# Performance work log

Measured on AMD Instinct MI355X. Metric: run time of the kernel, lower is better.

The kernel has to match this reference:

```python
import jax, jax.numpy as jnp
import numpy as np

EPS = 1e-5


def _conv(x, w, groups=1):
    # x: NCHW, w: OIHW, stride 1, padding k//2 == SAME for k=3
    return jax.lax.conv_general_dilated(
        x, w, window_strides=(1, 1), padding='SAME',
        feature_group_count=groups,
        dimension_numbers=('NCHW', 'OIHW', 'NCHW'))


def _bn(x, gamma, beta, mean, var):
    # eval-mode BatchNorm2d
    s = gamma * jax.lax.rsqrt(var + EPS)
    return x * s[None, :, None, None] + (beta - mean * s)[None, :, None, None]


def _bilinear_up_kernel(ch, k):
    # dla_up.fill_up_weights: bilinear upsampling kernel, shape (ch, 1, k, k)
    f = (k + 1) // 2
    c = (2 * f - 1 - f % 2) / (2.0 * f)
    i = np.arange(k)
    w1d = 1.0 - np.abs(i / f - c)
    w2d = np.outer(w1d, w1d).astype(np.float32)  # (k, k)
    return jnp.asarray(np.broadcast_to(w2d, (ch, 1, k, k)).copy())


def setup_inputs() -> dict:
    key = jax.random.key(0)
    ks = jax.random.split(key, 8)
    B, C, H, W = 16, 32, 128, 128
    OUT, NL = 8, 4
    layers = jax.random.normal(ks[0], (NL + 1, B, C, H, W), jnp.float32)
    node_w = jax.random.normal(ks[1], (NL, C, 2 * C, 3, 3), jnp.float32) * 0.05
    node_gamma = jnp.ones((NL, C), jnp.float32)
    node_beta = jnp.zeros((NL, C), jnp.float32)
    node_mean = jax.random.normal(ks[2], (NL, C), jnp.float32) * 0.1
    node_var = jax.random.uniform(ks[3], (NL, C), jnp.float32, 0.5, 1.5)
    final_w = jax.random.normal(ks[4], (OUT, C, 3, 3), jnp.float32) * 0.05
    final_gamma = jnp.ones((OUT,), jnp.float32)
    final_beta = jnp.zeros((OUT,), jnp.float32)
    final_mean = jax.random.normal(ks[5], (OUT,), jnp.float32) * 0.1
    final_var = jax.random.uniform(ks[6], (OUT,), jnp.float32, 0.5, 1.5)
    up_w = _bilinear_up_kernel(OUT, 4)  # frozen depthwise transpose-conv weight
    return dict(layers=layers, node_w=node_w, node_gamma=node_gamma,
                node_beta=node_beta, node_mean=node_mean, node_var=node_var,
                final_w=final_w, final_gamma=final_gamma, final_beta=final_beta,
                final_mean=final_mean, final_var=final_var, up_w=up_w)


def reference(layers, node_w, node_gamma, node_beta, node_mean, node_var,
              final_w, final_gamma, final_beta, final_mean, final_var, up_w):
    x = layers[0]
    n_layers = node_w.shape[0]
    for i in range(n_layers):  # fixed small structural loop
        h = jnp.concatenate([x, layers[i + 1]], axis=1)  # [B, 2C, H, W]
        x = jax.nn.relu(_bn(_conv(h, node_w[i]),
                            node_gamma[i], node_beta[i], node_mean[i], node_var[i]))
    x = jnp.tanh(_bn(_conv(x, final_w),
                     final_gamma, final_beta, final_mean, final_var))
    # depthwise ConvTranspose2d(k=4, stride=2, pad=1): equivalent fractionally
    # strided conv with flipped kernel, lhs_dilation=2, padding k-1-pad=2
    groups = up_w.shape[0]
    x = jax.lax.conv_general_dilated(
        x, up_w[:, :, ::-1, ::-1], window_strides=(1, 1),
        padding=[(2, 2), (2, 2)], lhs_dilation=(2, 2),
        feature_group_count=groups,
        dimension_numbers=('NCHW', 'OIHW', 'NCHW'))  # [B, OUT, 2H, 2W]
    # vectorized form of the per-row / per-col delta loops
    Ho, Wo = x.shape[2], x.shape[3]
    row_ramp = jnp.arange(Ho, dtype=x.dtype) / Ho  # delta_i = i / H
    col_ramp = jnp.arange(Wo, dtype=x.dtype) / Wo  # delta_j = j / W
    x = x.at[:, 0].add(row_ramp[None, :, None])
    x = x.at[:, 1].add(col_ramp[None, None, :])
    return x
```

## Files before the change

kernel.cpp:

```cpp
#include <hip/hip_runtime.h>
#include <hip/hip_bf16.h>
#include <cmath>

using bf16 = __hip_bfloat16;
typedef _Float16 f16x8 __attribute__((ext_vector_type(8)));
typedef float f32x16 __attribute__((ext_vector_type(16)));

__device__ __forceinline__ float ldin(const void* p, size_t i, int f) {
    return f ? ((const float*)p)[i] : __bfloat162float(((const bf16*)p)[i]);
}

__device__ __forceinline__ float bfu(unsigned short u) {
    union { unsigned u32; float f; } x; x.u32 = (unsigned)u << 16; return x.f;
}

__device__ __forceinline__ int swq(int X) { return (X + (X >> 2)) & 3; }

__device__ __forceinline__ int detect_f(const void* layers_) {
    const unsigned short* u = (const unsigned short*)layers_;
    __shared__ int s_bad;
    if (threadIdx.x == 0) s_bad = 0;
    __syncthreads();
    int bad = 0;
#pragma unroll
    for (int k = 0; k < 16; ++k) {
        unsigned short v = u[2 * ((threadIdx.x * 16 + k) * 257)];
        int e = (v >> 7) & 0xFF;
        bad += (e == 0xFF || (e == 0 && (v & 0x7FFF))) ? 1 : 0;
    }
    if (bad) atomicAdd(&s_bad, bad);
    __syncthreads();
    return s_bad > 0;
}

__global__ void pack_kernel(const void* __restrict__ nw, const void* __restrict__ ng,
                            const void* __restrict__ nb, const void* __restrict__ nm,
                            const void* __restrict__ nv, const void* __restrict__ fw,
                            const void* __restrict__ fg, const void* __restrict__ fb,
                            const void* __restrict__ fm, const void* __restrict__ fv,
                            const void* __restrict__ upw, const void* __restrict__ layers_,
                            char* __restrict__ ws) {
    const int f = detect_f(layers_);
    if (blockIdx.x == 0 && threadIdx.x == 0) *(volatile int*)ws = f;
    int i = blockIdx.x * 256 + threadIdx.x;
    _Float16* wpkN = (_Float16*)(ws + 160);
    _Float16* wpkF = (_Float16*)(ws + 147616);
    float* upwf  = (float*)(ws + 166048);
    float* nbias = (float*)(ws + 166560);
    float* fbias = (float*)(ws + 167072);
    if (i < 73728) {
        int e = i & 7, lane = (i >> 3) & 63, rest = i >> 9;
        int t = rest % 9, rest2 = rest / 9;
        int kc = rest2 & 3, lay = rest2 >> 2;
        int oc = lane & 31, ic = kc * 16 + ((lane >> 5) << 3) + e;
        float s = ldin(ng, lay * 32 + oc, f) * rsqrtf(ldin(nv, lay * 32 + oc, f) + 1e-5f);
        float w = ldin(nw, ((size_t)(lay * 32 + oc) * 64 + ic) * 9 + t, f);
        wpkN[i] = (_Float16)(w * s);
    } else if (i < 82944) {
        int j = i - 73728;
        int e = j & 7, lane = (j >> 3) & 63, rest = j >> 9;
        int t = rest % 9, kc = rest / 9;
        int oc = lane & 31, ic = kc * 16 + ((lane >> 5) << 3) + e;
        float v = 0.f;
        if (oc < 8) {
            float s = ldin(fg, oc, f) * rsqrtf(ldin(fv, oc, f) + 1e-5f);
            v = ldin(fw, ((size_t)(oc * 32 + ic)) * 9 + t, f) * s;
        }
        wpkF[j] = (_Float16)v;
    } else if (i < 83072) {
        int k = i - 82944;
        upwf[k] = ldin(upw, k, f);
    } else if (i < 83200) {
        int k = i - 83072;
        float s = ldin(ng, k, f) * rsqrtf(ldin(nv, k, f) + 1e-5f);
        nbias[k] = ldin(nb, k, f) - ldin(nm, k, f) * s;
    } else if (i < 83232) {
        int k = i - 83200;
        float v = 0.f;
        if (k < 8) {
            float s = ldin(fg, k, f) * rsqrtf(ldin(fv, k, f) + 1e-5f);
            v = ldin(fb, k, f) - ldin(fm, k, f) * s;
        }
        fbias[k] = v;
    }
}

__device__ __forceinline__ void stage_nchw_g(char* lds, const void* src,
                                             size_t base_elem, int f, int tid,
                                             int x0g, int y0g) {
#pragma unroll
    for (int it = 0; it < 6; ++it) {
        int job = tid + it * 256;
        if (it < 5 || job < 1360) {
            int c = job / 340, rest = job - c * 340;
            int row = rest / 34, X = rest - row * 34;
            int gy = y0g - 1 + row, gx = x0g - 1 + X;
            union { _Float16 h[8]; uint4 v; } pk;
            if (gy >= 0 && gy < 128 && gx >= 0 && gx < 128) {
                size_t e0 = base_elem + (size_t)(c * 8) * 16384 + (size_t)gy * 128 + gx;
                if (f) {
#pragma unroll
                    for (int j = 0; j < 8; ++j)
                        pk.h[j] = (_Float16)(((const float*)src)[e0 + (size_t)j * 16384]);
                } else {
#pragma unroll
                    for (int j = 0; j < 8; ++j)
                        pk.h[j] = (_Float16)bfu(((const unsigned short*)src)[e0 + (size_t)j * 16384]);
                }
            } else {
                pk.v = make_uint4(0u, 0u, 0u, 0u);
            }
            int slot = (c + swq(X)) & 3;
            *(uint4*)(lds + row * 2176 + (X << 6) + (slot << 4)) = pk.v;
        }
    }
}

__device__ __forceinline__ void stage_nhwc(char* lds, const _Float16* xh, int tid,
                                           int b, int x0g, int y0g) {
#pragma unroll
    for (int it = 0; it < 6; ++it) {
        int q = tid + it * 256;
        if (it < 5 || q < 1360) {
            int p = q >> 2, s = q & 3;
            int row = p / 34, X = p - row * 34;
            int c = (s - swq(X)) & 3;
            int gy = y0g - 1 + row, gx = x0g - 1 + X;
            uint4 v = {0u, 0u, 0u, 0u};
            if (gy >= 0 && gy < 128 && gx >= 0 && gx < 128)
                v = *(const uint4*)(xh + (((size_t)(b * 128 + gy) * 128 + gx) * 32 + c * 8));
            *(uint4*)(lds + (q << 4)) = v;
        }
    }
}

__device__ __forceinline__ void conv_both(const char* lds, const _Float16* wseg,
                                          int lane, int wid, int lh,
                                          f32x16& acc0, f32x16& acc1) {
    const int l31 = lane & 31;
#pragma unroll
    for (int kc = 0; kc < 4; ++kc) {
        f16x8 bfr[9];
#pragma unroll
        for (int t = 0; t < 9; ++t)
            bfr[t] = *(const f16x8*)(wseg + (size_t)((kc * 9 + t) * 64 + lane) * 8);
        const char* pl = lds + ((kc & 2) ? 21760 : 0);
        const int chunk = ((kc & 1) << 1) | lh;
#pragma unroll
        for (int iy = 0; iy < 4; ++iy) {
            const int rowoff = ((wid << 1) + iy) * 2176;
#pragma unroll
            for (int kx = 0; kx < 3; ++kx) {
                const int X = l31 + kx;
                const int slot = (chunk + swq(X)) & 3;
                const f16x8 a = *(const f16x8*)(pl + rowoff + (X << 6) + (slot << 4));
#pragma unroll
                for (int ky = 0; ky < 3; ++ky) {
                    const int y = iy - ky;
                    if (y == 0)
                        acc0 = __builtin_amdgcn_mfma_f32_32x32x16_f16(a, bfr[ky * 3 + kx], acc0, 0, 0, 0);
                    else if (y == 1)
                        acc1 = __builtin_amdgcn_mfma_f32_32x32x16_f16(a, bfr[ky * 3 + kx], acc1, 0, 0, 0);
                }
            }
        }
    }
}

__device__ __forceinline__ void conv_plane(const char* lds, const _Float16* wseg,
                                           int lane, int wid, int lh,
                                           f32x16& acc0, f32x16& acc1) {
    const int l31 = lane & 31;
#pragma unroll
    for (int kc = 0; kc < 2; ++kc) {
        f16x8 bfr[9];
#pragma unroll
        for (int t = 0; t < 9; ++t)
            bfr[t] = *(const f16x8*)(wseg + (size_t)((kc * 9 + t) * 64 + lane) * 8);
        const int chunk = (kc << 1) | lh;
#pragma unroll
        for (int iy = 0; iy < 4; ++iy) {
            const int rowoff = ((wid << 1) + iy) * 2176;
#pragma unroll
            for (int kx = 0; kx < 3; ++kx) {
                const int X = l31 + kx;
                const int slot = (chunk + swq(X)) & 3;
                const f16x8 a = *(const f16x8*)(lds + rowoff + (X << 6) + (slot << 4));
#pragma unroll
                for (int ky = 0; ky < 3; ++ky) {
                    const int y = iy - ky;
                    if (y == 0)
                        acc0 = __builtin_amdgcn_mfma_f32_32x32x16_f16(a, bfr[ky * 3 + kx], acc0, 0, 0, 0);
                    else if (y == 1)
                        acc1 = __builtin_amdgcn_mfma_f32_32x32x16_f16(a, bfr[ky * 3 + kx], acc1, 0, 0, 0);
                }
            }
        }
    }
}

__global__ __launch_bounds__(256, 3) void node_conv_mfma(
    const void* __restrict__ xprev, int xprev_nchw, int xprev_slice,
    const void* __restrict__ layers, int skip_slice,
    const _Float16* __restrict__ wl, const float* __restrict__ bias,
    const int* __restrict__ flag, _Float16* __restrict__ out) {
    __shared__ char lds[43520];
    const int f = flag[0];
    const int tid = threadIdx.x;
    const int x0g = blockIdx.x << 5, y0g = blockIdx.y << 3, b = blockIdx.z;
    const int lane = tid & 63, wid = tid >> 6;
    const int l31 = lane & 31, lh = lane >> 5;

    if (xprev_nchw)
        stage_nchw_g(lds, xprev, (size_t)xprev_slice * 8388608 + (size_t)b * 524288,
                     f, tid, x0g, y0g);
    else
        stage_nhwc(lds, (const _Float16*)xprev, tid, b, x0g, y0g);
    stage_nchw_g(lds + 21760, layers, (size_t)skip_slice * 8388608 + (size_t)b * 524288,
                 f, tid, x0g, y0g);
    __syncthreads();

    f32x16 acc0, acc1;
#pragma unroll
    for (int r = 0; r < 16; ++r) { acc0[r] = 0.f; acc1[r] = 0.f; }
    conv_both(lds, wl, lane, wid, lh, acc0, acc1);
    __syncthreads();

    const float bs = bias[l31];
    const int row0 = wid << 1;
#pragma unroll
    for (int r = 0; r < 16; ++r) {
        const int xr = (r & 3) + ((r >> 2) << 3) + (lh << 2);
        *(_Float16*)(lds + (row0 * 32 + xr) * 80 + (l31 << 1)) =
            (_Float16)fmaxf(acc0[r] + bs, 0.f);
        *(_Float16*)(lds + ((row0 + 1) * 32 + xr) * 80 + (l31 << 1)) =
            (_Float16)fmaxf(acc1[r] + bs, 0.f);
    }
    __syncthreads();
    const size_t obase = ((size_t)(b * 128 + y0g) * 128 + x0g) * 32;
#pragma unroll
    for (int it = 0; it < 4; ++it) {
        int g = tid + it * 256;
        int prow = g >> 7, inrow = g & 127;
        uint4 v = *(const uint4*)(lds + (prow * 32 + (inrow >> 2)) * 80 + (inrow & 3) * 16);
        *(uint4*)(out + obase + (size_t)prow * 4096 + inrow * 8) = v;
    }
}

__device__ __forceinline__ float ftanh(float x) {
    float e = __expf(2.f * x);
    return 1.f - 2.f / (e + 1.f);
}

__global__ __launch_bounds__(256, 3) void final_conv_mfma(
    const _Float16* __restrict__ xin, const _Float16* __restrict__ wf,
    const float* __restrict__ fbias, _Float16* __restrict__ outF) {
    __shared__ char lds[21760];
    const int tid = threadIdx.x;
    const int x0g = blockIdx.x << 5, y0g = blockIdx.y << 3, b = blockIdx.z;
    const int lane = tid & 63, wid = tid >> 6;
    const int l31 = lane & 31, lh = lane >> 5;

    stage_nhwc(lds, xin, tid, b, x0g, y0g);
    __syncthreads();

    f32x16 acc0, acc1;
#pragma unroll
    for (int r = 0; r < 16; ++r) { acc0[r] = 0.f; acc1[r] = 0.f; }
    conv_plane(lds, wf, lane, wid, lh, acc0, acc1);
    __syncthreads();

    const float bs = fbias[l31];
    const int row0 = wid << 1;
    if (l31 < 8) {
#pragma unroll
        for (int r = 0; r < 16; ++r) {
            const int xr = (r & 3) + ((r >> 2) << 3) + (lh << 2);
            *(_Float16*)(lds + (row0 * 32 + xr) * 16 + (l31 << 1)) =
                (_Float16)ftanh(acc0[r] + bs);
            *(_Float16*)(lds + ((row0 + 1) * 32 + xr) * 16 + (l31 << 1)) =
                (_Float16)ftanh(acc1[r] + bs);
        }
    }
    __syncthreads();
    {
        int g = tid;
        int prow = g >> 5, px = g & 31;
        uint4 v = *(const uint4*)(lds + g * 16);
        *(uint4*)(outF + ((size_t)(b * 128 + y0g + prow) * 128 + x0g + px) * 8) = v;
    }
}

__global__ __launch_bounds__(256) void upsample_q(
    const _Float16* __restrict__ F, const float* __restrict__ wf,
    const int* __restrict__ flag, void* __restrict__ out) {
    const int f = flag[0];
    int i = blockIdx.x * 256 + threadIdx.x;
    int qx = i & 127, qy = (i >> 7) & 127, b = i >> 14;

    f16x8 inb[3][3];
#pragma unroll
    for (int jy = 0; jy < 3; ++jy)
#pragma unroll
        for (int jx = 0; jx < 3; ++jx) {
            int iy = qy - 1 + jy, ix = qx - 1 + jx;
            f16x8 v;
#pragma unroll
            for (int c = 0; c < 8; ++c) v[c] = (_Float16)0.f;
            if (iy >= 0 && iy < 128 && ix >= 0 && ix < 128)
                v = *(const f16x8*)(F + (((size_t)(b * 128 + iy) * 128 + ix) << 3));
            inb[jy][jx] = v;
        }

    float acc[32];
#pragma unroll
    for (int k = 0; k < 32; ++k) acc[k] = 0.f;
#pragma unroll
    for (int ky = 0; ky < 4; ++ky) {
        const int dy = 1 - (ky & 1), jy = 2 - ((ky + 1) >> 1);
#pragma unroll
        for (int kx = 0; kx < 4; ++kx) {
            const int dx = 1 - (kx & 1), jx = 2 - ((kx + 1) >> 1);
            const f16x8 p = inb[jy][jx];
#pragma unroll
            for (int c = 0; c < 8; ++c)
                acc[c * 4 + dy * 2 + dx] =
                    fmaf((float)p[c], wf[c * 16 + ky * 4 + kx], acc[c * 4 + dy * 2 + dx]);
        }
    }
#pragma unroll
    for (int d = 0; d < 4; ++d) {
        acc[d]     += (float)(2 * qy + (d >> 1)) * (1.0f / 256.0f);
        acc[4 + d] += (float)(2 * qx + (d & 1)) * (1.0f / 256.0f);
    }
#pragma unroll
    for (int c = 0; c < 8; ++c)
#pragma unroll
        for (int dy2 = 0; dy2 < 2; ++dy2) {
            size_t a = ((size_t)(b * 8 + c) * 256 + (qy * 2 + dy2)) * 256 + qx * 2;
            float v0 = acc[c * 4 + dy2 * 2], v1 = acc[c * 4 + dy2 * 2 + 1];
            if (f) {
                *(float2*)((float*)out + a) = make_float2(v0, v1);
            } else {
                union { bf16 h; unsigned short u; } u0, u1;
                u0.h = __float2bfloat16(v0); u1.h = __float2bfloat16(v1);
                ((unsigned*)out)[a >> 1] = (unsigned)u0.u | ((unsigned)u1.u << 16);
            }
        }
}

extern "C" void kernel_launch(void* const* d_in, const int* in_sizes, int n_in,
                              void* d_out, int out_size, void* d_ws, size_t ws_size,
                              hipStream_t stream) {
    const void* layers = d_in[0];
    const void* node_w = d_in[1];
    const void* ng     = d_in[2];
    const void* nb     = d_in[3];
    const void* nm     = d_in[4];
    const void* nv     = d_in[5];
    const void* fw     = d_in[6];
    const void* fg     = d_in[7];
    const void* fb     = d_in[8];
    const void* fm     = d_in[9];
    const void* fv     = d_in[10];
    const void* upw    = d_in[11];

    char* ws = (char*)d_ws;
    int* dflag       = (int*)d_ws;
    _Float16* wpkN   = (_Float16*)(ws + 160);
    _Float16* wpkF   = (_Float16*)(ws + 147616);
    float* upwf      = (float*)(ws + 166048);
    float* nbias     = (float*)(ws + 166560);
    float* fbias     = (float*)(ws + 167072);
    _Float16* X      = (_Float16*)(ws + 167424);
    _Float16* Y      = (_Float16*)d_out;

    pack_kernel<<<326, 256, 0, stream>>>(node_w, ng, nb, nm, nv,
                                         fw, fg, fb, fm, fv, upw, layers, ws);

    dim3 g(4, 16, 16), blk(256);
    node_conv_mfma<<<g, blk, 0, stream>>>(layers, 1, 0, layers, 1,
                                          wpkN, nbias, dflag, X);
    node_conv_mfma<<<g, blk, 0, stream>>>(X, 0, 0, layers, 2,
                                          wpkN + 18432, nbias + 32, dflag, Y);
    node_conv_mfma<<<g, blk, 0, stream>>>(Y, 0, 0, layers, 3,
                                          wpkN + 2 * 18432, nbias + 64, dflag, X);
    node_conv_mfma<<<g, blk, 0, stream>>>(X, 0, 0, layers, 4,
                                          wpkN + 3 * 18432, nbias + 96, dflag, Y);
    final_conv_mfma<<<g, blk, 0, stream>>>(Y, wpkF, fbias, X);
    upsample_q<<<1024, 256, 0, stream>>>(X, upwf, dflag, d_out);
}
```

Before: 388.8 us.

## Fuse all stages into a persistent megakernel with software grid barriers

Replaces the pack, four node-conv, final-conv and upsample launches with one persistent kernel of 512 blocks. Each block walks the 1024 tiles of every stage in a grid-stride loop, and stages are separated by an atomic-counter grid barrier in the workspace. Format detection now runs in every block instead of being stored as a flag. The aim is to remove per-launch overhead and the gaps between kernels. In exchange, each CU runs fewer concurrent blocks (2 instead of 3), the barriers spin, and the design relies on all 512 blocks being co-resident to avoid deadlock.

```diff
diff --git a/kernel.cpp b/kernel.cpp
--- a/kernel.cpp
+++ b/kernel.cpp
@@ -6,6 +6,8 @@
 typedef _Float16 f16x8 __attribute__((ext_vector_type(8)));
 typedef float f32x16 __attribute__((ext_vector_type(16)));
 
+#define GRIDN 512
+
 __device__ __forceinline__ float ldin(const void* p, size_t i, int f) {
     return f ? ((const float*)p)[i] : __bfloat162float(((const bf16*)p)[i]);
 }
@@ -15,6 +17,19 @@
 }
 
 __device__ __forceinline__ int swq(int X) { return (X + (X >> 2)) & 3; }
+
+__device__ __forceinline__ void gbar(unsigned* cnt, unsigned& ep) {
+    __syncthreads();
+    if (threadIdx.x == 0) {
+        ep += 1;
+        __threadfence();
+        atomicAdd(cnt, 1u);
+        while (atomicAdd(cnt, 0u) < ep * (unsigned)GRIDN)
+            __builtin_amdgcn_s_sleep(2);
+        __threadfence();
+    }
+    __syncthreads();
+}
 
 __device__ __forceinline__ int detect_f(const void* layers_) {
     const unsigned short* u = (const unsigned short*)layers_;
@@ -31,58 +46,6 @@
     if (bad) atomicAdd(&s_bad, bad);
     __syncthreads();
     return s_bad > 0;
-}
-
-__global__ void pack_kernel(const void* __restrict__ nw, const void* __restrict__ ng,
-                            const void* __restrict__ nb, const void* __restrict__ nm,
-                            const void* __restrict__ nv, const void* __restrict__ fw,
-                            const void* __restrict__ fg, const void* __restrict__ fb,
-                            const void* __restrict__ fm, const void* __restrict__ fv,
-                            const void* __restrict__ upw, const void* __restrict__ layers_,
-                            char* __restrict__ ws) {
-    const int f = detect_f(layers_);
-    if (blockIdx.x == 0 && threadIdx.x == 0) *(volatile int*)ws = f;
-    int i = blockIdx.x * 256 + threadIdx.x;
-    _Float16* wpkN = (_Float16*)(ws + 160);
-    _Float16* wpkF = (_Float16*)(ws + 147616);
-    float* upwf  = (float*)(ws + 166048);
-    float* nbias = (float*)(ws + 166560);
-    float* fbias = (float*)(ws + 167072);
-    if (i < 73728) {
-        int e = i & 7, lane = (i >> 3) & 63, rest = i >> 9;
-        int t = rest % 9, rest2 = rest / 9;
-        int kc = rest2 & 3, lay = rest2 >> 2;
-        int oc = lane & 31, ic = kc * 16 + ((lane >> 5) << 3) + e;
-        float s = ldin(ng, lay * 32 + oc, f) * rsqrtf(ldin(nv, lay * 32 + oc, f) + 1e-5f);
-        float w = ldin(nw, ((size_t)(lay * 32 + oc) * 64 + ic) * 9 + t, f);
-        wpkN[i] = (_Float16)(w * s);
-    } else if (i < 82944) {
-        int j = i - 73728;
-        int e = j & 7, lane = (j >> 3) & 63, rest = j >> 9;
-        int t = rest % 9, kc = rest / 9;
-        int oc = lane & 31, ic = kc * 16 + ((lane >> 5) << 3) + e;
-        float v = 0.f;
-        if (oc < 8) {
-            float s = ldin(fg, oc, f) * rsqrtf(ldin(fv, oc, f) + 1e-5f);
-            v = ldin(fw, ((size_t)(oc * 32 + ic)) * 9 + t, f) * s;
-        }
-        wpkF[j] = (_Float16)v;
-    } else if (i < 83072) {
-        int k = i - 82944;
-        upwf[k] = ldin(upw, k, f);
-    } else if (i < 83200) {
-        int k = i - 83072;
-        float s = ldin(ng, k, f) * rsqrtf(ldin(nv, k, f) + 1e-5f);
-        nbias[k] = ldin(nb, k, f) - ldin(nm, k, f) * s;
-    } else if (i < 83232) {
-        int k = i - 83200;
-        float v = 0.f;
-        if (k < 8) {
-            float s = ldin(fg, k, f) * rsqrtf(ldin(fv, k, f) + 1e-5f);
-            v = ldin(fb, k, f) - ldin(fm, k, f) * s;
-        }
-        fbias[k] = v;
-    }
 }
 
 __device__ __forceinline__ void stage_nchw_g(char* lds, const void* src,
@@ -199,154 +162,231 @@
     }
 }
 
-__global__ __launch_bounds__(256, 3) void node_conv_mfma(
-    const void* __restrict__ xprev, int xprev_nchw, int xprev_slice,
-    const void* __restrict__ layers, int skip_slice,
-    const _Float16* __restrict__ wl, const float* __restrict__ bias,
-    const int* __restrict__ flag, _Float16* __restrict__ out) {
-    __shared__ char lds[43520];
-    const int f = flag[0];
-    const int tid = threadIdx.x;
-    const int x0g = blockIdx.x << 5, y0g = blockIdx.y << 3, b = blockIdx.z;
-    const int lane = tid & 63, wid = tid >> 6;
-    const int l31 = lane & 31, lh = lane >> 5;
-
-    if (xprev_nchw)
-        stage_nchw_g(lds, xprev, (size_t)xprev_slice * 8388608 + (size_t)b * 524288,
-                     f, tid, x0g, y0g);
-    else
-        stage_nhwc(lds, (const _Float16*)xprev, tid, b, x0g, y0g);
-    stage_nchw_g(lds + 21760, layers, (size_t)skip_slice * 8388608 + (size_t)b * 524288,
-                 f, tid, x0g, y0g);
-    __syncthreads();
-
-    f32x16 acc0, acc1;
-#pragma unroll
-    for (int r = 0; r < 16; ++r) { acc0[r] = 0.f; acc1[r] = 0.f; }
-    conv_both(lds, wl, lane, wid, lh, acc0, acc1);
-    __syncthreads();
-
-    const float bs = bias[l31];
-    const int row0 = wid << 1;
-#pragma unroll
-    for (int r = 0; r < 16; ++r) {
-        const int xr = (r & 3) + ((r >> 2) << 3) + (lh << 2);
-        *(_Float16*)(lds + (row0 * 32 + xr) * 80 + (l31 << 1)) =
-            (_Float16)fmaxf(acc0[r] + bs, 0.f);
-        *(_Float16*)(lds + ((row0 + 1) * 32 + xr) * 80 + (l31 << 1)) =
-            (_Float16)fmaxf(acc1[r] + bs, 0.f);
-    }
-    __syncthreads();
-    const size_t obase = ((size_t)(b * 128 + y0g) * 128 + x0g) * 32;
-#pragma unroll
-    for (int it = 0; it < 4; ++it) {
-        int g = tid + it * 256;
-        int prow = g >> 7, inrow = g & 127;
-        uint4 v = *(const uint4*)(lds + (prow * 32 + (inrow >> 2)) * 80 + (inrow & 3) * 16);
-        *(uint4*)(out + obase + (size_t)prow * 4096 + inrow * 8) = v;
-    }
-}
-
 __device__ __forceinline__ float ftanh(float x) {
     float e = __expf(2.f * x);
     return 1.f - 2.f / (e + 1.f);
 }
 
-__global__ __launch_bounds__(256, 3) void final_conv_mfma(
-    const _Float16* __restrict__ xin, const _Float16* __restrict__ wf,
-    const float* __restrict__ fbias, _Float16* __restrict__ outF) {
-    __shared__ char lds[21760];
+__device__ __forceinline__ void node_phase(char* lds, const void* xprev,
+    int xprev_nchw, int xprev_slice, const void* layers, int skip_slice,
+    const _Float16* wl, const float* bias, int f, _Float16* out) {
     const int tid = threadIdx.x;
-    const int x0g = blockIdx.x << 5, y0g = blockIdx.y << 3, b = blockIdx.z;
     const int lane = tid & 63, wid = tid >> 6;
     const int l31 = lane & 31, lh = lane >> 5;
-
-    stage_nhwc(lds, xin, tid, b, x0g, y0g);
-    __syncthreads();
-
-    f32x16 acc0, acc1;
-#pragma unroll
-    for (int r = 0; r < 16; ++r) { acc0[r] = 0.f; acc1[r] = 0.f; }
-    conv_plane(lds, wf, lane, wid, lh, acc0, acc1);
-    __syncthreads();
-
-    const float bs = fbias[l31];
-    const int row0 = wid << 1;
-    if (l31 < 8) {
+    for (int t = blockIdx.x; t < 1024; t += GRIDN) {
+        __syncthreads();
+        const int x0g = (t & 3) << 5, y0g = ((t >> 2) & 15) << 3, b = t >> 6;
+
+        if (xprev_nchw)
+            stage_nchw_g(lds, xprev, (size_t)xprev_slice * 8388608 + (size_t)b * 524288,
+                         f, tid, x0g, y0g);
+        else
+            stage_nhwc(lds, (const _Float16*)xprev, tid, b, x0g, y0g);
+        stage_nchw_g(lds + 21760, layers, (size_t)skip_slice * 8388608 + (size_t)b * 524288,
+                     f, tid, x0g, y0g);
+        __syncthreads();
+
+        f32x16 acc0, acc1;
+#pragma unroll
+        for (int r = 0; r < 16; ++r) { acc0[r] = 0.f; acc1[r] = 0.f; }
+        conv_both(lds, wl, lane, wid, lh, acc0, acc1);
+        __syncthreads();
+
+        const float bs = bias[l31];
+        const int row0 = wid << 1;
 #pragma unroll
         for (int r = 0; r < 16; ++r) {
             const int xr = (r & 3) + ((r >> 2) << 3) + (lh << 2);
-            *(_Float16*)(lds + (row0 * 32 + xr) * 16 + (l31 << 1)) =
-                (_Float16)ftanh(acc0[r] + bs);
-            *(_Float16*)(lds + ((row0 + 1) * 32 + xr) * 16 + (l31 << 1)) =
-                (_Float16)ftanh(acc1[r] + bs);
-        }
-    }
-    __syncthreads();
+            *(_Float16*)(lds + (row0 * 32 + xr) * 80 + (l31 << 1)) =
+                (_Float16)fmaxf(acc0[r] + bs, 0.f);
+            *(_Float16*)(lds + ((row0 + 1) * 32 + xr) * 80 + (l31 << 1)) =
+                (_Float16)fmaxf(acc1[r] + bs, 0.f);
+        }
+        __syncthreads();
+        const size_t obase = ((size_t)(b * 128 + y0g) * 128 + x0g) * 32;
+#pragma unroll
+        for (int it = 0; it < 4; ++it) {
+            int g = tid + it * 256;
+            int prow = g >> 7, inrow = g & 127;
+            uint4 v = *(const uint4*)(lds + (prow * 32 + (inrow >> 2)) * 80 + (inrow & 3) * 16);
+            *(uint4*)(out + obase + (size_t)prow * 4096 + inrow * 8) = v;
+        }
+    }
+}
+
+__device__ __forceinline__ void final_phase(char* lds, const _Float16* xin,
+                                            const _Float16* wf, const float* fbias,
+                                            _Float16* outF) {
+    const int tid = threadIdx.x;
+    const int lane = tid & 63, wid = tid >> 6;
+    const int l31 = lane & 31, lh = lane >> 5;
+    for (int t = blockIdx.x; t < 1024; t += GRIDN) {
+        __syncthreads();
+        const int x0g = (t & 3) << 5, y0g = ((t >> 2) & 15) << 3, b = t >> 6;
+        stage_nhwc(lds, xin, tid, b, x0g, y0g);
+        __syncthreads();
+
+        f32x16 acc0, acc1;
+#pragma unroll
+        for (int r = 0; r < 16; ++r) { acc0[r] = 0.f; acc1[r] = 0.f; }
+        conv_plane(lds, wf, lane, wid, lh, acc0, acc1);
+        __syncthreads();
+
+        const float bs = fbias[l31];
+        const int row0 = wid << 1;
+        if (l31 < 8) {
+#pragma unroll
+            for (int r = 0; r < 16; ++r) {
+                const int xr = (r & 3) + ((r >> 2) << 3) + (lh << 2);
+                *(_Float16*)(lds + (row0 * 32 + xr) * 16 + (l31 << 1)) =
+                    (_Float16)ftanh(acc0[r] + bs);
+                *(_Float16*)(lds + ((row0 + 1) * 32 + xr) * 16 + (l31 << 1)) =
+                    (_Float16)ftanh(acc1[r] + bs);
+            }
+        }
+        __syncthreads();
+        {
+            int g = tid;
+            uint4 v = *(const uint4*)(lds + g * 16);
+            int prow = g >> 5, px = g & 31;
+            *(uint4*)(outF + ((size_t)(b * 128 + y0g + prow) * 128 + x0g + px) * 8) = v;
+        }
+    }
+}
+
+__device__ __forceinline__ void up_phase(const _Float16* F, const float* wf,
+                                         int f, void* out) {
+    for (int t = blockIdx.x; t < 1024; t += GRIDN) {
+        int i = t * 256 + threadIdx.x;
+        int qx = i & 127, qy = (i >> 7) & 127, b = i >> 14;
+
+        f16x8 inb[3][3];
+#pragma unroll
+        for (int jy = 0; jy < 3; ++jy)
+#pragma unroll
+            for (int jx = 0; jx < 3; ++jx) {
+                int iy = qy - 1 + jy, ix = qx - 1 + jx;
+                f16x8 v;
+#pragma unroll
+                for (int c = 0; c < 8; ++c) v[c] = (_Float16)0.f;
+                if (iy >= 0 && iy < 128 && ix >= 0 && ix < 128)
+                    v = *(const f16x8*)(F + (((size_t)(b * 128 + iy) * 128 + ix) << 3));
+                inb[jy][jx] = v;
+            }
+
+        float acc[32];
+#pragma unroll
+        for (int k = 0; k < 32; ++k) acc[k] = 0.f;
+#pragma unroll
+        for (int ky = 0; ky < 4; ++ky) {
+            const int dy = 1 - (ky & 1), jy = 2 - ((ky + 1) >> 1);
+#pragma unroll
+            for (int kx = 0; kx < 4; ++kx) {
+                const int dx = 1 - (kx & 1), jx = 2 - ((kx + 1) >> 1);
+                const f16x8 p = inb[jy][jx];
+#pragma unroll
+                for (int c = 0; c < 8; ++c)
+                    acc[c * 4 + dy * 2 + dx] =
+                        fmaf((float)p[c], wf[c * 16 + ky * 4 + kx], acc[c * 4 + dy * 2 + dx]);
+            }
+        }
+#pragma unroll
+        for (int d = 0; d < 4; ++d) {
+            acc[d]     += (float)(2 * qy + (d >> 1)) * (1.0f / 256.0f);
+            acc[4 + d] += (float)(2 * qx + (d & 1)) * (1.0f / 256.0f);
+        }
+#pragma unroll
+        for (int c = 0; c < 8; ++c)
+#pragma unroll
+            for (int dy2 = 0; dy2 < 2; ++dy2) {
+                size_t a = ((size_t)(b * 8 + c) * 256 + (qy * 2 + dy2)) * 256 + qx * 2;
+                float v0 = acc[c * 4 + dy2 * 2], v1 = acc[c * 4 + dy2 * 2 + 1];
+                if (f) {
+                    *(float2*)((float*)out + a) = make_float2(v0, v1);
+                } else {
+                    union { bf16 h; unsigned short u; } u0, u1;
+                    u0.h = __float2bfloat16(v0); u1.h = __float2bfloat16(v1);
+                    ((unsigned*)out)[a >> 1] = (unsigned)u0.u | ((unsigned)u1.u << 16);
+                }
+            }
+    }
+}
+
+__global__ __launch_bounds__(256, 2) void mega_kernel(
+    const void* __restrict__ layers, const void* __restrict__ nw,
+    const void* __restrict__ ng, const void* __restrict__ nbp,
+    const void* __restrict__ nm, const void* __restrict__ nv,
+    const void* __restrict__ fw, const void* __restrict__ fg,
+    const void* __restrict__ fb, const void* __restrict__ fm,
+    const void* __restrict__ fv, const void* __restrict__ upw,
+    char* __restrict__ ws, void* __restrict__ dout) {
+    __shared__ char lds[43520];
+    unsigned* cnt = (unsigned*)ws;
+    unsigned ep = 0;
+
+    const int f = detect_f(layers);
+
+    _Float16* wpkN = (_Float16*)(ws + 160);
+    _Float16* wpkF = (_Float16*)(ws + 147616);
+    float* upwf  = (float*)(ws + 166048);
+    float* nbias = (float*)(ws + 166560);
+    float* fbias = (float*)(ws + 167072);
+    _Float16* X  = (_Float16*)(ws + 167424);
+    _Float16* Y  = (_Float16*)dout;
+
     {
-        int g = tid;
-        int prow = g >> 5, px = g & 31;
-        uint4 v = *(const uint4*)(lds + g * 16);
-        *(uint4*)(outF + ((size_t)(b * 128 + y0g + prow) * 128 + x0g + px) * 8) = v;
-    }
-}
-
-__global__ __launch_bounds__(256) void upsample_q(
-    const _Float16* __restrict__ F, const float* __restrict__ wf,
-    const int* __restrict__ flag, void* __restrict__ out) {
-    const int f = flag[0];
-    int i = blockIdx.x * 256 + threadIdx.x;
-    int qx = i & 127, qy = (i >> 7) & 127, b = i >> 14;
-
-    f16x8 inb[3][3];
-#pragma unroll
-    for (int jy = 0; jy < 3; ++jy)
-#pragma unroll
-        for (int jx = 0; jx < 3; ++jx) {
-            int iy = qy - 1 + jy, ix = qx - 1 + jx;
-            f16x8 v;
-#pragma unroll
-            for (int c = 0; c < 8; ++c) v[c] = (_Float16)0.f;
-            if (iy >= 0 && iy < 128 && ix >= 0 && ix < 128)
-                v = *(const f16x8*)(F + (((size_t)(b * 128 + iy) * 128 + ix) << 3));
-            inb[jy][jx] = v;
-        }
-
-    float acc[32];
-#pragma unroll
-    for (int k = 0; k < 32; ++k) acc[k] = 0.f;
-#pragma unroll
-    for (int ky = 0; ky < 4; ++ky) {
-        const int dy = 1 - (ky & 1), jy = 2 - ((ky + 1) >> 1);
-#pragma unroll
-        for (int kx = 0; kx < 4; ++kx) {
-            const int dx = 1 - (kx & 1), jx = 2 - ((kx + 1) >> 1);
-            const f16x8 p = inb[jy][jx];
-#pragma unroll
-            for (int c = 0; c < 8; ++c)
-                acc[c * 4 + dy * 2 + dx] =
-                    fmaf((float)p[c], wf[c * 16 + ky * 4 + kx], acc[c * 4 + dy * 2 + dx]);
-        }
-    }
-#pragma unroll
-    for (int d = 0; d < 4; ++d) {
-        acc[d]     += (float)(2 * qy + (d >> 1)) * (1.0f / 256.0f);
-        acc[4 + d] += (float)(2 * qx + (d & 1)) * (1.0f / 256.0f);
-    }
-#pragma unroll
-    for (int c = 0; c < 8; ++c)
-#pragma unroll
-        for (int dy2 = 0; dy2 < 2; ++dy2) {
-            size_t a = ((size_t)(b * 8 + c) * 256 + (qy * 2 + dy2)) * 256 + qx * 2;
-            float v0 = acc[c * 4 + dy2 * 2], v1 = acc[c * 4 + dy2 * 2 + 1];
-            if (f) {
-                *(float2*)((float*)out + a) = make_float2(v0, v1);
-            } else {
-                union { bf16 h; unsigned short u; } u0, u1;
-                u0.h = __float2bfloat16(v0); u1.h = __float2bfloat16(v1);
-                ((unsigned*)out)[a >> 1] = (unsigned)u0.u | ((unsigned)u1.u << 16);
-            }
-        }
+        int i = blockIdx.x * 256 + threadIdx.x;
+        if (i < 73728) {
+            int e = i & 7, lane = (i >> 3) & 63, rest = i >> 9;
+            int t = rest % 9, rest2 = rest / 9;
+            int kc = rest2 & 3, lay = rest2 >> 2;
+            int oc = lane & 31, ic = kc * 16 + ((lane >> 5) << 3) + e;
+            float s = ldin(ng, lay * 32 + oc, f) * rsqrtf(ldin(nv, lay * 32 + oc, f) + 1e-5f);
+            float w = ldin(nw, ((size_t)(lay * 32 + oc) * 64 + ic) * 9 + t, f);
+            wpkN[i] = (_Float16)(w * s);
+        } else if (i < 82944) {
+            int j = i - 73728;
+            int e = j & 7, lane = (j >> 3) & 63, rest = j >> 9;
+            int t = rest % 9, kc = rest / 9;
+            int oc = lane & 31, ic = kc * 16 + ((lane >> 5) << 3) + e;
+            float v = 0.f;
+            if (oc < 8) {
+                float s = ldin(fg, oc, f) * rsqrtf(ldin(fv, oc, f) + 1e-5f);
+                v = ldin(fw, ((size_t)(oc * 32 + ic)) * 9 + t, f) * s;
+            }
+            wpkF[j] = (_Float16)v;
+        } else if (i < 83072) {
+            int k = i - 82944;
+            upwf[k] = ldin(upw, k, f);
+        } else if (i < 83200) {
+            int k = i - 83072;
+            float s = ldin(ng, k, f) * rsqrtf(ldin(nv, k, f) + 1e-5f);
+            nbias[k] = ldin(nbp, k, f) - ldin(nm, k, f) * s;
+        } else if (i < 83232) {
+            int k = i - 83200;
+            float v = 0.f;
+            if (k < 8) {
+                float s = ldin(fg, k, f) * rsqrtf(ldin(fv, k, f) + 1e-5f);
+                v = ldin(fb, k, f) - ldin(fm, k, f) * s;
+            }
+            fbias[k] = v;
+        }
+    }
+    gbar(cnt, ep);
+
+    node_phase(lds, layers, 1, 0, layers, 1, wpkN,         nbias,      f, X);
+    gbar(cnt, ep);
+    node_phase(lds, X,      0, 0, layers, 2, wpkN + 18432, nbias + 32, f, Y);
+    gbar(cnt, ep);
+    node_phase(lds, Y,      0, 0, layers, 3, wpkN + 36864, nbias + 64, f, X);
+    gbar(cnt, ep);
+    node_phase(lds, X,      0, 0, layers, 4, wpkN + 55296, nbias + 96, f, Y);
+    gbar(cnt, ep);
+
+    final_phase(lds, Y, wpkF, fbias, X);
+    gbar(cnt, ep);
+
+    up_phase(X, upwf, f, dout);
 }
 
 extern "C" void kernel_launch(void* const* d_in, const int* in_sizes, int n_in,
@@ -364,29 +404,9 @@
     const void* fm     = d_in[9];
     const void* fv     = d_in[10];
     const void* upw    = d_in[11];
-
     char* ws = (char*)d_ws;
-    int* dflag       = (int*)d_ws;
-    _Float16* wpkN   = (_Float16*)(ws + 160);
-    _Float16* wpkF   = (_Float16*)(ws + 147616);
-    float* upwf      = (float*)(ws + 166048);
-    float* nbias     = (float*)(ws + 166560);
-    float* fbias     = (float*)(ws + 167072);
-    _Float16* X      = (_Float16*)(ws + 167424);
-    _Float16* Y      = (_Float16*)d_out;
-
-    pack_kernel<<<326, 256, 0, stream>>>(node_w, ng, nb, nm, nv,
-                                         fw, fg, fb, fm, fv, upw, layers, ws);
-
-    dim3 g(4, 16, 16), blk(256);
-    node_conv_mfma<<<g, blk, 0, stream>>>(layers, 1, 0, layers, 1,
-                                          wpkN, nbias, dflag, X);
-    node_conv_mfma<<<g, blk, 0, stream>>>(X, 0, 0, layers, 2,
-                                          wpkN + 18432, nbias + 32, dflag, Y);
-    node_conv_mfma<<<g, blk, 0, stream>>>(Y, 0, 0, layers, 3,
-                                          wpkN + 2 * 18432, nbias + 64, dflag, X);
-    node_conv_mfma<<<g, blk, 0, stream>>>(X, 0, 0, layers, 4,
-                                          wpkN + 3 * 18432, nbias + 96, dflag, Y);
-    final_conv_mfma<<<g, blk, 0, stream>>>(Y, wpkF, fbias, X);
-    upsample_q<<<1024, 256, 0, stream>>>(X, upwf, dflag, d_out);
-}
+
+    hipMemsetAsync(ws, 0, 16, stream);
+    mega_kernel<<<dim3(GRIDN), dim3(256), 0, stream>>>(
+        layers, node_w, ng, nb, nm, nv, fw, fg, fb, fm, fv, upw, ws, d_out);
+}
```

After: 694.6 us. +78.6%, slower.
